# Performance work log

Hardware: AMD Instinct MI355X
Metric: run time of the kernel (lower is better)

## Reference

```python
import jax, jax.numpy as jnp
import numpy as np

B, D, E, H = 2048, 1024, 32, 1024  # tokens, hidden, total experts (m*N), ffn_dim_small


def setup_inputs() -> dict:
    key = jax.random.key(0)
    ks = jax.random.split(key, 5)
    scale_in = 1.0 / np.sqrt(D)
    scale_h = 1.0 / np.sqrt(H)
    return {
        "x": jax.random.normal(ks[0], (B, D), dtype=jnp.float32),
        "Wg": jax.random.normal(ks[1], (D, E), dtype=jnp.float32) * scale_in,
        "W1": jax.random.normal(ks[2], (E, D, H), dtype=jnp.float32) * scale_in,
        "b1": jnp.zeros((E, H), dtype=jnp.float32),
        "W2": jax.random.normal(ks[3], (E, H, D), dtype=jnp.float32) * scale_h,
        "b2": jnp.zeros((E, D), dtype=jnp.float32),
        "topk": 8,  # m * K
    }


def reference(x, Wg, W1, b1, W2, b2, topk):
    # gating: softmax then keep only top-k probs (others zeroed), no renorm
    logits = x @ Wg                                   # [B, E]
    probs = jax.nn.softmax(logits, axis=-1)           # [B, E]
    _, idx = jax.lax.top_k(probs, topk)               # [B, topk]
    mask = jnp.zeros_like(probs).at[jnp.arange(x.shape[0])[:, None], idx].set(1.0)
    gate = probs * mask                               # [B, E]

    # dense all-expert FFN (faithful to original which runs every expert)
    h = jax.nn.relu(jnp.einsum('bd,edh->beh', x, W1) + b1)   # [B, E, H]
    y = jnp.einsum('beh,ehd->bed', h, W2) + b2               # [B, E, D]

    moe_out = jnp.einsum('be,bed->bd', gate, y)              # weighted sum over experts
    return x + moe_out
```

## Files before the change

kernel.cpp:

```cpp
#include <hip/hip_runtime.h>
#include <hip/hip_bf16.h>

#define B_TOK 2048
#define DDIM 1024
#define NEXP 32
#define HDIM 1024
#define TOPK 8
#define PITCH 1040

typedef __bf16 bf16_t;
typedef __bf16 bf16x8 __attribute__((ext_vector_type(8)));
typedef float f32x4 __attribute__((ext_vector_type(4)));

__global__ __launch_bounds__(256) void k_prep(const float* __restrict__ x,
                                              bf16_t* __restrict__ xb,
                                              float* __restrict__ out) {
  int i = (blockIdx.x * 256 + threadIdx.x) * 8;
  float4 v0 = *(const float4*)&x[i];
  float4 v1 = *(const float4*)&x[i + 4];
  bf16x8 v;
  v[0] = (bf16_t)v0.x; v[1] = (bf16_t)v0.y; v[2] = (bf16_t)v0.z; v[3] = (bf16_t)v0.w;
  v[4] = (bf16_t)v1.x; v[5] = (bf16_t)v1.y; v[6] = (bf16_t)v1.z; v[7] = (bf16_t)v1.w;
  int row = i >> 10, col = i & 1023;
  *(bf16x8*)&xb[(size_t)row * PITCH + col] = v;
  *(float4*)&out[i] = v0;
  *(float4*)&out[i + 4] = v1;
}

__global__ __launch_bounds__(256) void k_gating(const float* __restrict__ x,
                                                const float* __restrict__ Wg,
                                                int* __restrict__ sel_e,
                                                float* __restrict__ sel_w) {
  int token = blockIdx.x * 4 + (threadIdx.x >> 6);
  int lane = threadIdx.x & 63;
  int e = lane & 31;
  int half = lane >> 5;
  const float* xr = x + (size_t)token * DDIM + half * (DDIM / 2);
  const float* wg = Wg + (size_t)half * (DDIM / 2) * NEXP + e;
  float acc = 0.f;
#pragma unroll 8
  for (int k = 0; k < DDIM / 2; ++k) acc = fmaf(xr[k], wg[k * NEXP], acc);
  acc += __shfl_xor(acc, 32);
  float m = acc;
  for (int off = 16; off; off >>= 1) m = fmaxf(m, __shfl_xor(m, off));
  float p = __expf(acc - m);
  float s = p;
  for (int off = 16; off; off >>= 1) s += __shfl_xor(s, off);
  p /= s;
  float pv = p;
  int my_se = 0;
  float my_sw = 0.f;
  for (int it = 0; it < TOPK; ++it) {
    float mx = pv;
    for (int off = 16; off; off >>= 1) mx = fmaxf(mx, __shfl_xor(mx, off));
    unsigned long long bal = __ballot(pv == mx);
    int sl = __ffsll(bal) - 1;
    int se = sl & 31;
    if (lane == it) { my_se = se; my_sw = mx; }
    if (e == se) pv = -1.f;
  }
  if (lane < TOPK) {
    sel_e[token * TOPK + lane] = my_se;
    sel_w[token * TOPK + lane] = my_sw;
  }
}

__global__ __launch_bounds__(256) void k_build_lists(const int* __restrict__ sel_e,
                                                     const float* __restrict__ sel_w,
                                                     int* __restrict__ list,
                                                     float* __restrict__ wlist,
                                                     int* __restrict__ count) {
  int e = blockIdx.x;
  int t = threadIdx.x;
  int lane = t & 63, wv = t >> 6;
  __shared__ int wsum[4];
  __shared__ int base;
  if (t == 0) base = 0;
  __syncthreads();
  for (int c = 0; c < B_TOK; c += 256) {
    int b = c + t;
    int flag = 0, slot = 0;
    float w = 0.f;
#pragma unroll
    for (int j = 0; j < TOPK; ++j) {
      if (sel_e[b * TOPK + j] == e) { flag = 1; slot = j; w = sel_w[b * TOPK + j]; }
    }
    unsigned long long bal = __ballot(flag);
    int pre = __popcll(bal & ((1ull << lane) - 1ull));
    int tot = __popcll(bal);
    if (lane == 0) wsum[wv] = tot;
    __syncthreads();
    int off = base;
    for (int i = 0; i < wv; ++i) off += wsum[i];
    if (flag) {
      int pos = off + pre;
      list[e * B_TOK + pos] = (b << 3) | slot;
      wlist[e * B_TOK + pos] = w;
    }
    __syncthreads();
    if (t == 0) base += wsum[0] + wsum[1] + wsum[2] + wsum[3];
    __syncthreads();
  }
  if (t == 0) count[e] = base;
}

__global__ __launch_bounds__(64) void k_build_queue(const int* __restrict__ count,
                                                    int* __restrict__ queue,
                                                    int* __restrict__ qn) {
  int e = threadIdx.x;
  int nmt = 0;
  if (e < NEXP) nmt = (count[e] + 127) >> 7;
  int pref = 0, tot = 0;
  for (int i = 0; i < NEXP; ++i) {
    int v = __shfl(nmt, i);
    if (i < e) pref += v;
    tot += v;
  }
  if (e < NEXP) {
    int base = pref * 8;
    for (int y = 0; y < 8; ++y)
      for (int mt = 0; mt < nmt; ++mt)
        queue[base + y * nmt + mt] = (e << 8) | (mt << 3) | y;
  }
  if (threadIdx.x == 0) qn[0] = tot * 8;
}

__global__ __launch_bounds__(256) void k_transpose(const float* __restrict__ W1,
                                                   const float* __restrict__ W2,
                                                   bf16_t* __restrict__ W1t,
                                                   bf16_t* __restrict__ W2t) {
  __shared__ bf16_t tile[64 * 128];
  int z = blockIdx.z;
  const float* in;
  bf16_t* out;
  if (z < NEXP) {
    in = W1 + (size_t)z * DDIM * HDIM;
    out = W1t + (size_t)z * HDIM * PITCH;
  } else {
    in = W2 + (size_t)(z - NEXP) * DDIM * HDIM;
    out = W2t + (size_t)(z - NEXP) * DDIM * PITCH;
  }
  const int n0 = blockIdx.x * 64;
  const int k0 = blockIdx.y * 128;
  const int t = threadIdx.x;
  const int k8 = (t >> 4) * 8;
  const int n4 = (t & 15) * 4;

  float4 v[8];
#pragma unroll
  for (int kk = 0; kk < 8; ++kk)
    v[kk] = *(const float4*)&in[(size_t)(k0 + k8 + kk) * 1024 + n0 + n4];

#pragma unroll
  for (int jn = 0; jn < 4; ++jn) {
    const int n = n4 + jn;
    bf16x8 p;
#pragma unroll
    for (int kk = 0; kk < 8; ++kk) p[kk] = (bf16_t)(((const float*)&v[kk])[jn]);
    const int pu = (k8 >> 3) ^ ((n >> 2) & 15);
    *(bf16x8*)&tile[n * 128 + pu * 8] = p;
  }
  __syncthreads();

  const int cw = t & 15;
#pragma unroll
  for (int r2 = 0; r2 < 4; ++r2) {
    const int n = (t >> 4) + r2 * 16;
    const int pu = cw ^ ((n >> 2) & 15);
    uint4 val = *(const uint4*)&tile[n * 128 + pu * 8];
    *(uint4*)&out[(size_t)(n0 + n) * PITCH + k0 + cw * 8] = val;
  }
}

__device__ __forceinline__ void async_load16(const bf16_t* g, bf16_t* l) {
  __builtin_amdgcn_global_load_lds((const __attribute__((address_space(1))) void*)g,
                                   (__attribute__((address_space(3))) void*)l, 16, 0, 0);
}

template <int PHASE>
__global__ __launch_bounds__(256, 3) void k_gemm(const bf16_t* __restrict__ Abase,
                                                 const bf16_t* __restrict__ Bt,
                                                 const int* __restrict__ list,
                                                 const float* __restrict__ wlist,
                                                 const int* __restrict__ count,
                                                 const int* __restrict__ queue,
                                                 const int* __restrict__ qn,
                                                 const float* __restrict__ bias,
                                                 bf16_t* __restrict__ hbuf,
                                                 float* __restrict__ out) {
  __shared__ bf16_t As[128][64];
  __shared__ bf16_t Bs[128][64];

  const int phys = blockIdx.x;
  const int nwg = qn[0];
  if (phys >= nwg) return;
  const int q8 = nwg >> 3, r8 = nwg & 7;
  const int xcd = phys & 7, loc = phys >> 3;
  const int wk = (xcd < r8 ? xcd * (q8 + 1) : r8 * (q8 + 1) + (xcd - r8) * q8) + loc;

  const int ent = queue[wk];
  const int e = ent >> 8;
  const int mt = (ent >> 3) & 31;
  const int y = ent & 7;

  const int cnt = count[e];
  const int m0 = mt * 128;
  const int n0 = y * 128;

  const int t = threadIdx.x;
  const int lane = t & 63;
  const int w = t >> 6;
  const int wm = (w >> 1) << 6;
  const int wc = (w & 1) << 6;
  const int lr = lane & 15;
  const int hi = lane >> 4;
  const int l7 = lane & 7;
  const int srs = ((lane & 7) ^ (lane >> 3)) << 3;

  const int* lrow = list + e * B_TOK;

  const bf16_t* aptr[4];
#pragma unroll
  for (int i = 0; i < 4; ++i) {
    int mi = m0 + w * 32 + i * 8 + (lane >> 3);
    if (mi > cnt - 1) mi = cnt - 1;
    int li = lrow[mi];
    int tok = li >> 3, slot = li & 7;
    size_t arow = (PHASE == 1) ? (size_t)tok * PITCH : ((size_t)tok * 8 + slot) * PITCH;
    aptr[i] = Abase + arow + srs;
  }
  const bf16_t* bptr[4];
#pragma unroll
  for (int i = 0; i < 4; ++i)
    bptr[i] = Bt + ((size_t)e * 1024 + n0 + w * 32 + i * 8 + (lane >> 3)) * PITCH + srs;

  f32x4 acc[4][4] = {};

#pragma unroll 1
  for (int kt = 0; kt < 16; ++kt) {
#pragma unroll
    for (int i = 0; i < 4; ++i) {
      async_load16(aptr[i] + kt * 64, &As[w * 32 + i * 8][0]);
      async_load16(bptr[i] + kt * 64, &Bs[w * 32 + i * 8][0]);
    }
    __syncthreads();
    bf16x8 af[4][2], bfr[4][2];
#pragma unroll
    for (int ks = 0; ks < 2; ++ks) {
      const int ca = (((ks << 2) | hi) ^ l7) << 3;
#pragma unroll
      for (int m = 0; m < 4; ++m)
        af[m][ks] = *(const bf16x8*)&As[wm + m * 16 + lr][ca];
#pragma unroll
      for (int n = 0; n < 4; ++n)
        bfr[n][ks] = *(const bf16x8*)&Bs[wc + n * 16 + lr][ca];
    }
#pragma unroll
    for (int m = 0; m < 4; ++m)
#pragma unroll
      for (int n = 0; n < 4; ++n)
#pragma unroll
        for (int ks = 0; ks < 2; ++ks)
          acc[m][n] = __builtin_amdgcn_mfma_f32_16x16x32_bf16(af[m][ks], bfr[n][ks], acc[m][n], 0, 0, 0);
    __syncthreads();
  }

  float biasv[4];
#pragma unroll
  for (int n = 0; n < 4; ++n) biasv[n] = bias[e * 1024 + n0 + wc + n * 16 + lr];

#pragma unroll
  for (int m = 0; m < 4; ++m) {
#pragma unroll
    for (int j = 0; j < 4; ++j) {
      int gm = m0 + wm + m * 16 + hi * 4 + j;
      if (gm < cnt) {
        int li2 = lrow[gm];
        int tok2 = li2 >> 3, slot2 = li2 & 7;
        if (PHASE == 1) {
          bf16_t* hr = hbuf + ((size_t)tok2 * 8 + slot2) * PITCH + n0 + wc + lr;
#pragma unroll
          for (int n = 0; n < 4; ++n) {
            float v = acc[m][n][j] + biasv[n];
            hr[n * 16] = (bf16_t)(v > 0.f ? v : 0.f);
          }
        } else {
          float gw = wlist[e * B_TOK + gm];
          float* orow = out + (size_t)tok2 * DDIM + n0 + wc + lr;
#pragma unroll
          for (int n = 0; n < 4; ++n) {
            float v = (acc[m][n][j] + biasv[n]) * gw;
            unsafeAtomicAdd(&orow[n * 16], v);
          }
        }
      }
    }
  }
}

extern "C" void kernel_launch(void* const* d_in, const int* in_sizes, int n_in,
                              void* d_out, int out_size, void* d_ws, size_t ws_size,
                              hipStream_t stream) {
  const float* x = (const float*)d_in[0];
  const float* Wg = (const float*)d_in[1];
  const float* W1 = (const float*)d_in[2];
  const float* b1 = (const float*)d_in[3];
  const float* W2 = (const float*)d_in[4];
  const float* b2 = (const float*)d_in[5];
  float* out = (float*)d_out;

  char* ws = (char*)d_ws;
  bf16_t* xb = (bf16_t*)ws;   ws += (size_t)B_TOK * PITCH * 2;
  bf16_t* W1t = (bf16_t*)ws;  ws += (size_t)NEXP * HDIM * PITCH * 2;
  bf16_t* W2t = (bf16_t*)ws;  ws += (size_t)NEXP * DDIM * PITCH * 2;
  bf16_t* hbuf = (bf16_t*)ws; ws += (size_t)B_TOK * TOPK * PITCH * 2;
  int* sel_e = (int*)ws;      ws += (size_t)B_TOK * TOPK * 4;
  float* sel_w = (float*)ws;  ws += (size_t)B_TOK * TOPK * 4;
  int* list = (int*)ws;       ws += (size_t)NEXP * B_TOK * 4;
  float* wlist = (float*)ws;  ws += (size_t)NEXP * B_TOK * 4;
  int* count = (int*)ws;      ws += 64 * 4;
  int* queue = (int*)ws;      ws += 2048 * 4;
  int* qn = (int*)ws;         ws += 64 * 4;

  k_prep<<<1024, 256, 0, stream>>>(x, xb, out);
  k_gating<<<512, 256, 0, stream>>>(x, Wg, sel_e, sel_w);
  k_build_lists<<<32, 256, 0, stream>>>(sel_e, sel_w, list, wlist, count);
  k_build_queue<<<1, 64, 0, stream>>>(count, queue, qn);
  k_transpose<<<dim3(16, 8, 64), 256, 0, stream>>>(W1, W2, W1t, W2t);
  k_gemm<1><<<1536, 256, 0, stream>>>(xb, W1t, list, wlist, count, queue, qn, b1, hbuf, out);
  k_gemm<2><<<1536, 256, 0, stream>>>(hbuf, W2t, list, wlist, count, queue, qn, b2, hbuf, out);
}
```

Before: 300.5 us.

## Widen expert GEMM tiles to 128x256 and enlarge transpose tiles

The grouped expert GEMMs now compute a 128x256 output tile per workgroup (each wave 64x128) instead of 128x128, which halves the number of work items and reloads of the gathered A rows. The queue encoding, grid sizes and launch bounds (occupancy 3 to 2) are adjusted to match. The weight transpose kernel also moves to larger 128x256 tiles with a wider XOR swizzle. The cost is more registers and LDS per workgroup, lower occupancy, and fewer workgroups, which can hurt load balance for experts with few tokens.

Result: slower. 324.2 us (+7.9%).

```diff
diff --git a/kernel.cpp b/kernel.cpp
--- a/kernel.cpp
+++ b/kernel.cpp
@@ -117,19 +117,19 @@
     tot += v;
   }
   if (e < NEXP) {
-    int base = pref * 8;
-    for (int y = 0; y < 8; ++y)
+    int base = pref * 4;
+    for (int y = 0; y < 4; ++y)
       for (int mt = 0; mt < nmt; ++mt)
-        queue[base + y * nmt + mt] = (e << 8) | (mt << 3) | y;
-  }
-  if (threadIdx.x == 0) qn[0] = tot * 8;
+        queue[base + y * nmt + mt] = (e << 8) | (mt << 2) | y;
+  }
+  if (threadIdx.x == 0) qn[0] = tot * 4;
 }
 
 __global__ __launch_bounds__(256) void k_transpose(const float* __restrict__ W1,
                                                    const float* __restrict__ W2,
                                                    bf16_t* __restrict__ W1t,
                                                    bf16_t* __restrict__ W2t) {
-  __shared__ bf16_t tile[64 * 128];
+  __shared__ bf16_t tile[128 * 256];
   int z = blockIdx.z;
   const float* in;
   bf16_t* out;
@@ -140,35 +140,39 @@
     in = W2 + (size_t)(z - NEXP) * DDIM * HDIM;
     out = W2t + (size_t)(z - NEXP) * DDIM * PITCH;
   }
-  const int n0 = blockIdx.x * 64;
-  const int k0 = blockIdx.y * 128;
+  const int n0 = blockIdx.x * 128;
+  const int k0 = blockIdx.y * 256;
   const int t = threadIdx.x;
-  const int k8 = (t >> 4) * 8;
-  const int n4 = (t & 15) * 4;
-
-  float4 v[8];
-#pragma unroll
-  for (int kk = 0; kk < 8; ++kk)
-    v[kk] = *(const float4*)&in[(size_t)(k0 + k8 + kk) * 1024 + n0 + n4];
-
-#pragma unroll
-  for (int jn = 0; jn < 4; ++jn) {
-    const int n = n4 + jn;
-    bf16x8 p;
-#pragma unroll
-    for (int kk = 0; kk < 8; ++kk) p[kk] = (bf16_t)(((const float*)&v[kk])[jn]);
-    const int pu = (k8 >> 3) ^ ((n >> 2) & 15);
-    *(bf16x8*)&tile[n * 128 + pu * 8] = p;
+  const int g = t >> 5;
+  const int c = t & 31;
+
+#pragma unroll
+  for (int ab = 0; ab < 4; ++ab) {
+    const int kb = ab * 64 + g * 8;
+    float4 v[8];
+#pragma unroll
+    for (int kk = 0; kk < 8; ++kk)
+      v[kk] = *(const float4*)&in[(size_t)(k0 + kb + kk) * 1024 + n0 + c * 4];
+    const int u = ab * 8 + g;
+#pragma unroll
+    for (int jn = 0; jn < 4; ++jn) {
+      const int n = c * 4 + jn;
+      bf16x8 p;
+#pragma unroll
+      for (int kk = 0; kk < 8; ++kk) p[kk] = (bf16_t)(((const float*)&v[kk])[jn]);
+      const int phys = u ^ ((n >> 2) & 31);
+      *(bf16x8*)&tile[n * 256 + phys * 8] = p;
+    }
   }
   __syncthreads();
 
-  const int cw = t & 15;
-#pragma unroll
-  for (int r2 = 0; r2 < 4; ++r2) {
-    const int n = (t >> 4) + r2 * 16;
-    const int pu = cw ^ ((n >> 2) & 15);
-    uint4 val = *(const uint4*)&tile[n * 128 + pu * 8];
-    *(uint4*)&out[(size_t)(n0 + n) * PITCH + k0 + cw * 8] = val;
+#pragma unroll
+  for (int it = 0; it < 16; ++it) {
+    const int n = (t >> 5) + it * 8;
+    const int phys = c ^ ((n >> 2) & 31);
+    uint4 val = *(const uint4*)&tile[n * 256 + phys * 8];
+    const int koff = (c >> 3) * 64 + (c & 7) * 8;
+    *(uint4*)&out[(size_t)(n0 + n) * PITCH + k0 + koff] = val;
   }
 }
 
@@ -178,7 +182,7 @@
 }
 
 template <int PHASE>
-__global__ __launch_bounds__(256, 3) void k_gemm(const bf16_t* __restrict__ Abase,
+__global__ __launch_bounds__(256, 2) void k_gemm(const bf16_t* __restrict__ Abase,
                                                  const bf16_t* __restrict__ Bt,
                                                  const int* __restrict__ list,
                                                  const float* __restrict__ wlist,
@@ -189,7 +193,7 @@
                                                  bf16_t* __restrict__ hbuf,
                                                  float* __restrict__ out) {
   __shared__ bf16_t As[128][64];
-  __shared__ bf16_t Bs[128][64];
+  __shared__ bf16_t Bs[256][64];
 
   const int phys = blockIdx.x;
   const int nwg = qn[0];
@@ -200,18 +204,18 @@
 
   const int ent = queue[wk];
   const int e = ent >> 8;
-  const int mt = (ent >> 3) & 31;
-  const int y = ent & 7;
+  const int mt = (ent >> 2) & 0x3F;
+  const int y = ent & 3;
 
   const int cnt = count[e];
   const int m0 = mt * 128;
-  const int n0 = y * 128;
+  const int n0 = y * 256;
 
   const int t = threadIdx.x;
   const int lane = t & 63;
   const int w = t >> 6;
   const int wm = (w >> 1) << 6;
-  const int wc = (w & 1) << 6;
+  const int wc = (w & 1) << 7;
   const int lr = lane & 15;
   const int hi = lane >> 4;
   const int l7 = lane & 7;
@@ -229,45 +233,70 @@
     size_t arow = (PHASE == 1) ? (size_t)tok * PITCH : ((size_t)tok * 8 + slot) * PITCH;
     aptr[i] = Abase + arow + srs;
   }
-  const bf16_t* bptr[4];
-#pragma unroll
-  for (int i = 0; i < 4; ++i)
-    bptr[i] = Bt + ((size_t)e * 1024 + n0 + w * 32 + i * 8 + (lane >> 3)) * PITCH + srs;
-
-  f32x4 acc[4][4] = {};
+  const bf16_t* bptr[8];
+#pragma unroll
+  for (int i = 0; i < 8; ++i)
+    bptr[i] = Bt + ((size_t)e * 1024 + n0 + w * 64 + i * 8 + (lane >> 3)) * PITCH + srs;
+
+  f32x4 acc[4][8] = {};
 
 #pragma unroll 1
   for (int kt = 0; kt < 16; ++kt) {
 #pragma unroll
-    for (int i = 0; i < 4; ++i) {
+    for (int i = 0; i < 4; ++i)
       async_load16(aptr[i] + kt * 64, &As[w * 32 + i * 8][0]);
-      async_load16(bptr[i] + kt * 64, &Bs[w * 32 + i * 8][0]);
-    }
-    __syncthreads();
-    bf16x8 af[4][2], bfr[4][2];
+#pragma unroll
+    for (int i = 0; i < 8; ++i)
+      async_load16(bptr[i] + kt * 64, &Bs[w * 64 + i * 8][0]);
+    __syncthreads();
+    bf16x8 af[4][2];
 #pragma unroll
     for (int ks = 0; ks < 2; ++ks) {
       const int ca = (((ks << 2) | hi) ^ l7) << 3;
 #pragma unroll
       for (int m = 0; m < 4; ++m)
         af[m][ks] = *(const bf16x8*)&As[wm + m * 16 + lr][ca];
-#pragma unroll
-      for (int n = 0; n < 4; ++n)
-        bfr[n][ks] = *(const bf16x8*)&Bs[wc + n * 16 + lr][ca];
-    }
-#pragma unroll
-    for (int m = 0; m < 4; ++m)
-#pragma unroll
-      for (int n = 0; n < 4; ++n)
-#pragma unroll
-        for (int ks = 0; ks < 2; ++ks)
-          acc[m][n] = __builtin_amdgcn_mfma_f32_16x16x32_bf16(af[m][ks], bfr[n][ks], acc[m][n], 0, 0, 0);
-    __syncthreads();
-  }
-
-  float biasv[4];
-#pragma unroll
-  for (int n = 0; n < 4; ++n) biasv[n] = bias[e * 1024 + n0 + wc + n * 16 + lr];
+    }
+    {
+      bf16x8 bfr[4][2];
+#pragma unroll
+      for (int ks = 0; ks < 2; ++ks) {
+        const int ca = (((ks << 2) | hi) ^ l7) << 3;
+#pragma unroll
+        for (int n = 0; n < 4; ++n)
+          bfr[n][ks] = *(const bf16x8*)&Bs[wc + n * 16 + lr][ca];
+      }
+#pragma unroll
+      for (int m = 0; m < 4; ++m)
+#pragma unroll
+        for (int n = 0; n < 4; ++n)
+#pragma unroll
+          for (int ks = 0; ks < 2; ++ks)
+            acc[m][n] = __builtin_amdgcn_mfma_f32_16x16x32_bf16(af[m][ks], bfr[n][ks], acc[m][n], 0, 0, 0);
+    }
+    {
+      bf16x8 bfr[4][2];
+#pragma unroll
+      for (int ks = 0; ks < 2; ++ks) {
+        const int ca = (((ks << 2) | hi) ^ l7) << 3;
+#pragma unroll
+        for (int n = 0; n < 4; ++n)
+          bfr[n][ks] = *(const bf16x8*)&Bs[wc + 64 + n * 16 + lr][ca];
+      }
+#pragma unroll
+      for (int m = 0; m < 4; ++m)
+#pragma unroll
+        for (int n = 0; n < 4; ++n)
+#pragma unroll
+          for (int ks = 0; ks < 2; ++ks)
+            acc[m][4 + n] = __builtin_amdgcn_mfma_f32_16x16x32_bf16(af[m][ks], bfr[n][ks], acc[m][4 + n], 0, 0, 0);
+    }
+    __syncthreads();
+  }
+
+  float biasv[8];
+#pragma unroll
+  for (int n = 0; n < 8; ++n) biasv[n] = bias[e * 1024 + n0 + wc + n * 16 + lr];
 
 #pragma unroll
   for (int m = 0; m < 4; ++m) {
@@ -280,7 +309,7 @@
         if (PHASE == 1) {
           bf16_t* hr = hbuf + ((size_t)tok2 * 8 + slot2) * PITCH + n0 + wc + lr;
 #pragma unroll
-          for (int n = 0; n < 4; ++n) {
+          for (int n = 0; n < 8; ++n) {
             float v = acc[m][n][j] + biasv[n];
             hr[n * 16] = (bf16_t)(v > 0.f ? v : 0.f);
           }
@@ -288,7 +317,7 @@
           float gw = wlist[e * B_TOK + gm];
           float* orow = out + (size_t)tok2 * DDIM + n0 + wc + lr;
 #pragma unroll
-          for (int n = 0; n < 4; ++n) {
+          for (int n = 0; n < 8; ++n) {
             float v = (acc[m][n][j] + biasv[n]) * gw;
             unsafeAtomicAdd(&orow[n * 16], v);
           }
@@ -326,7 +355,7 @@
   k_gating<<<512, 256, 0, stream>>>(x, Wg, sel_e, sel_w);
   k_build_lists<<<32, 256, 0, stream>>>(sel_e, sel_w, list, wlist, count);
   k_build_queue<<<1, 64, 0, stream>>>(count, queue, qn);
-  k_transpose<<<dim3(16, 8, 64), 256, 0, stream>>>(W1, W2, W1t, W2t);
-  k_gemm<1><<<1536, 256, 0, stream>>>(xb, W1t, list, wlist, count, queue, qn, b1, hbuf, out);
-  k_gemm<2><<<1536, 256, 0, stream>>>(hbuf, W2t, list, wlist, count, queue, qn, b2, hbuf, out);
-}
+  k_transpose<<<dim3(8, 4, 64), 256, 0, stream>>>(W1, W2, W1t, W2t);
+  k_gemm<1><<<768, 256, 0, stream>>>(xb, W1t, list, wlist, count, queue, qn, b1, hbuf, out);
+  k_gemm<2><<<768, 256, 0, stream>>>(hbuf, W2t, list, wlist, count, queue, qn, b2, hbuf, out);
+}
```

## Fuse weight transpose and bf16 conversion into expert GEMM B-tile loads

Applied to the files above, without the earlier changes.

Drops the separate kernel that transposed and converted every expert's W1/W2 to bf16. The GEMM now reads fp32 weights directly, converts them in registers and writes swizzled bf16 tiles into shared memory. This removes a full pass over 256MB of fp32 weights plus the bf16 write, but each B tile is now re-read in fp32 by every M-tile of an expert, and those loads are synchronous instead of async-to-LDS. The activation pitch also changes.

Measured after the change: 268.2 us. 10.8% less time.

```diff
diff --git a/kernel.cpp b/kernel.cpp
--- a/kernel.cpp
+++ b/kernel.cpp
@@ -6,7 +6,7 @@
 #define NEXP 32
 #define HDIM 1024
 #define TOPK 8
-#define PITCH 1040
+#define PITCH 1088
 
 typedef __bf16 bf16_t;
 typedef __bf16 bf16x8 __attribute__((ext_vector_type(8)));
@@ -125,53 +125,6 @@
   if (threadIdx.x == 0) qn[0] = tot * 8;
 }
 
-__global__ __launch_bounds__(256) void k_transpose(const float* __restrict__ W1,
-                                                   const float* __restrict__ W2,
-                                                   bf16_t* __restrict__ W1t,
-                                                   bf16_t* __restrict__ W2t) {
-  __shared__ bf16_t tile[64 * 128];
-  int z = blockIdx.z;
-  const float* in;
-  bf16_t* out;
-  if (z < NEXP) {
-    in = W1 + (size_t)z * DDIM * HDIM;
-    out = W1t + (size_t)z * HDIM * PITCH;
-  } else {
-    in = W2 + (size_t)(z - NEXP) * DDIM * HDIM;
-    out = W2t + (size_t)(z - NEXP) * DDIM * PITCH;
-  }
-  const int n0 = blockIdx.x * 64;
-  const int k0 = blockIdx.y * 128;
-  const int t = threadIdx.x;
-  const int k8 = (t >> 4) * 8;
-  const int n4 = (t & 15) * 4;
-
-  float4 v[8];
-#pragma unroll
-  for (int kk = 0; kk < 8; ++kk)
-    v[kk] = *(const float4*)&in[(size_t)(k0 + k8 + kk) * 1024 + n0 + n4];
-
-#pragma unroll
-  for (int jn = 0; jn < 4; ++jn) {
-    const int n = n4 + jn;
-    bf16x8 p;
-#pragma unroll
-    for (int kk = 0; kk < 8; ++kk) p[kk] = (bf16_t)(((const float*)&v[kk])[jn]);
-    const int pu = (k8 >> 3) ^ ((n >> 2) & 15);
-    *(bf16x8*)&tile[n * 128 + pu * 8] = p;
-  }
-  __syncthreads();
-
-  const int cw = t & 15;
-#pragma unroll
-  for (int r2 = 0; r2 < 4; ++r2) {
-    const int n = (t >> 4) + r2 * 16;
-    const int pu = cw ^ ((n >> 2) & 15);
-    uint4 val = *(const uint4*)&tile[n * 128 + pu * 8];
-    *(uint4*)&out[(size_t)(n0 + n) * PITCH + k0 + cw * 8] = val;
-  }
-}
-
 __device__ __forceinline__ void async_load16(const bf16_t* g, bf16_t* l) {
   __builtin_amdgcn_global_load_lds((const __attribute__((address_space(1))) void*)g,
                                    (__attribute__((address_space(3))) void*)l, 16, 0, 0);
@@ -179,7 +132,7 @@
 
 template <int PHASE>
 __global__ __launch_bounds__(256, 3) void k_gemm(const bf16_t* __restrict__ Abase,
-                                                 const bf16_t* __restrict__ Bt,
+                                                 const float* __restrict__ Wraw,
                                                  const int* __restrict__ list,
                                                  const float* __restrict__ wlist,
                                                  const int* __restrict__ count,
@@ -229,19 +182,32 @@
     size_t arow = (PHASE == 1) ? (size_t)tok * PITCH : ((size_t)tok * 8 + slot) * PITCH;
     aptr[i] = Abase + arow + srs;
   }
-  const bf16_t* bptr[4];
-#pragma unroll
-  for (int i = 0; i < 4; ++i)
-    bptr[i] = Bt + ((size_t)e * 1024 + n0 + w * 32 + i * 8 + (lane >> 3)) * PITCH + srs;
+
+  const int cB = t & 31;
+  const int aB = t >> 5;
+  const float* bcol = Wraw + (size_t)e * DDIM * HDIM + n0 + cB * 4;
 
   f32x4 acc[4][4] = {};
 
 #pragma unroll 1
   for (int kt = 0; kt < 16; ++kt) {
 #pragma unroll
-    for (int i = 0; i < 4; ++i) {
+    for (int i = 0; i < 4; ++i)
       async_load16(aptr[i] + kt * 64, &As[w * 32 + i * 8][0]);
-      async_load16(bptr[i] + kt * 64, &Bs[w * 32 + i * 8][0]);
+    {
+      const float* p = bcol + (size_t)(kt * 64 + aB * 8) * 1024;
+      float4 v[8];
+#pragma unroll
+      for (int kk = 0; kk < 8; ++kk)
+        v[kk] = *(const float4*)(p + (size_t)kk * 1024);
+#pragma unroll
+      for (int jn = 0; jn < 4; ++jn) {
+        const int n = cB * 4 + jn;
+        bf16x8 pk;
+#pragma unroll
+        for (int kk = 0; kk < 8; ++kk) pk[kk] = (bf16_t)(((const float*)&v[kk])[jn]);
+        *(bf16x8*)&Bs[n][(aB ^ (n & 7)) << 3] = pk;
+      }
     }
     __syncthreads();
     bf16x8 af[4][2], bfr[4][2];
@@ -311,8 +277,6 @@
 
   char* ws = (char*)d_ws;
   bf16_t* xb = (bf16_t*)ws;   ws += (size_t)B_TOK * PITCH * 2;
-  bf16_t* W1t = (bf16_t*)ws;  ws += (size_t)NEXP * HDIM * PITCH * 2;
-  bf16_t* W2t = (bf16_t*)ws;  ws += (size_t)NEXP * DDIM * PITCH * 2;
   bf16_t* hbuf = (bf16_t*)ws; ws += (size_t)B_TOK * TOPK * PITCH * 2;
   int* sel_e = (int*)ws;      ws += (size_t)B_TOK * TOPK * 4;
   float* sel_w = (float*)ws;  ws += (size_t)B_TOK * TOPK * 4;
@@ -326,7 +290,6 @@
   k_gating<<<512, 256, 0, stream>>>(x, Wg, sel_e, sel_w);
   k_build_lists<<<32, 256, 0, stream>>>(sel_e, sel_w, list, wlist, count);
   k_build_queue<<<1, 64, 0, stream>>>(count, queue, qn);
-  k_transpose<<<dim3(16, 8, 64), 256, 0, stream>>>(W1, W2, W1t, W2t);
-  k_gemm<1><<<1536, 256, 0, stream>>>(xb, W1t, list, wlist, count, queue, qn, b1, hbuf, out);
-  k_gemm<2><<<1536, 256, 0, stream>>>(hbuf, W2t, list, wlist, count, queue, qn, b2, hbuf, out);
-}
+  k_gemm<1><<<1536, 256, 0, stream>>>(xb, W1, list, wlist, count, queue, qn, b1, hbuf, out);
+  k_gemm<2><<<1536, 256, 0, stream>>>(hbuf, W2, list, wlist, count, queue, qn, b2, hbuf, out);
+}
```
